# Kernel tuning notes

Hardware: AMD Instinct MI355X
Metric: run time of the kernel (lower is better)

Reference implementation:

```python
import jax, jax.numpy as jnp
import numpy as np

EPS = 1e-13

def masked_softmax(scores, mask):
    # scores: [B, L1, L2], mask: [B, L2] binary float
    # ESIM-style: softmax(scores * mask) * mask, renormalized.
    m = mask[:, None, :]                      # [B, 1, L2]
    r = jax.nn.softmax(scores * m, axis=-1) * m
    return r / (r.sum(axis=-1, keepdims=True) + EPS)

def weighted_sum(attn, tensor, mask):
    # attn: [B, L1, L2], tensor: [B, L2, D], mask: [B, L1]
    return jnp.matmul(attn, tensor) * mask[:, :, None]

def setup_inputs() -> dict:
    key = jax.random.key(0)
    k1, k2, k3, k4 = jax.random.split(key, 4)
    B, Lp, Lh, D = 64, 512, 512, 600
    encoded_premise = jax.random.normal(k1, (B, Lp, D), dtype=jnp.float32)
    encoded_hypothesis = jax.random.normal(k2, (B, Lh, D), dtype=jnp.float32)
    # binary padding masks (1 = valid token)
    premise_mask = (jax.random.uniform(k3, (B, Lp)) > 0.15).astype(jnp.float32)
    hypothesis_mask = (jax.random.uniform(k4, (B, Lh)) > 0.15).astype(jnp.float32)
    return {"encoded_premise": encoded_premise, "premise_mask": premise_mask,
            "encoded_hypothesis": encoded_hypothesis, "hypothesis_mask": hypothesis_mask}

def reference(encoded_premise, premise_mask, encoded_hypothesis, hypothesis_mask):
    # shared cross-attention score matrix [B, Lp, Lh]
    attn = jnp.einsum('bpd,bhd->bph', encoded_premise, encoded_hypothesis)
    a_p = masked_softmax(attn, hypothesis_mask)                    # [B, Lp, Lh]
    a_h = masked_softmax(attn.transpose(0, 2, 1), premise_mask)    # [B, Lh, Lp]
    weighted_premise = weighted_sum(a_p, encoded_hypothesis, premise_mask)      # [B, Lp, D]
    weighted_hypothesis = weighted_sum(a_h, encoded_premise, hypothesis_mask)   # [B, Lh, D]
    return (weighted_premise, weighted_hypothesis)
```

## Files before the change

### kernel.cpp

```cpp
#include <hip/hip_runtime.h>
#include <hip/hip_bf16.h>

#define DEVB 64
#define LSEQ 512
#define DDIM 600

typedef short short8 __attribute__((ext_vector_type(8)));
typedef float f32x4 __attribute__((ext_vector_type(4)));
typedef _Float16 f16x8 __attribute__((ext_vector_type(8)));
typedef _Float16 f16x4 __attribute__((ext_vector_type(4)));

constexpr int LDP = 40;

__device__ __forceinline__ unsigned short f2bf(float x) {
    union { float f; unsigned u; } v; v.f = x;
    unsigned r = v.u + 0x7fffu + ((v.u >> 16) & 1u);
    return (unsigned short)(r >> 16);
}
__device__ __forceinline__ f32x4 mfma16(short8 a, short8 b, f32x4 c) {
    return __builtin_amdgcn_mfma_f32_16x16x32_bf16(a, b, c, 0, 0, 0);
}
__device__ __forceinline__ f32x4 mfma16h(f16x8 a, f16x8 b, f32x4 c) {
    return __builtin_amdgcn_mfma_f32_16x16x32_f16(a, b, c, 0, 0, 0);
}

__global__ __launch_bounds__(256) void transcvt2(
    const float* __restrict__ P, const float* __restrict__ H,
    _Float16* __restrict__ pT, _Float16* __restrict__ hT)
{
    int blk = blockIdx.x;
    const float* X; _Float16* XT;
    if (blk < DEVB * 80) { X = P; XT = pT; }
    else { blk -= DEVB * 80; X = H; XT = hT; }

    int b   = blk / 80;
    int rem = blk % 80;
    int r0  = (rem / 10) << 6;
    int d0  = (rem % 10) << 6;
    const float* Xb = X + (size_t)b * LSEQ * DDIM;

    __shared__ _Float16 T[64 * 66];
    int t = threadIdx.x;
#pragma unroll
    for (int it = 0; it < 2; ++it) {
        int g  = t + (it << 8);
        int ri = g >> 3;
        int dc = (g & 7) << 3;
        if (d0 + dc < DDIM) {
            const float* src = Xb + (size_t)(r0 + ri) * DDIM + d0 + dc;
            float4 x0 = *(const float4*)src;
            float4 x1 = *(const float4*)(src + 4);
            float xf[8] = {x0.x, x0.y, x0.z, x0.w, x1.x, x1.y, x1.z, x1.w};
#pragma unroll
            for (int j = 0; j < 8; ++j)
                T[(dc + j) * 66 + ri] = (_Float16)xf[j];
        }
    }
    __syncthreads();

    int d  = t >> 2;
    int ch = (t & 3) << 4;
    if (d0 + d < DDIM) {
        unsigned buf[8];
#pragma unroll
        for (int i = 0; i < 8; ++i)
            buf[i] = *(const unsigned*)&T[d * 66 + ch + 2 * i];
        unsigned* dst = (unsigned*)(XT + ((size_t)b * DDIM + d0 + d) * LSEQ + r0 + ch);
        *(uint4*)(dst)     = *(uint4*)&buf[0];
        *(uint4*)(dst + 4) = *(uint4*)&buf[4];
    }
}

__global__ __launch_bounds__(256) void attn_gemm(
    const float* __restrict__ P, const float* __restrict__ H,
    float* __restrict__ attn)
{
    const int bid = blockIdx.x;
    const int swz = (bid & 7) * 128 + (bid >> 3);
    const int b  = swz >> 4;
    const int pt = ((swz >> 2) & 3) << 7;
    const int ht = (swz & 3) << 7;
    const float* Pb = P + ((size_t)b * LSEQ + pt) * DDIM;
    const float* Hb = H + ((size_t)b * LSEQ + ht) * DDIM;
    float* Ab = attn + (size_t)b * LSEQ * LSEQ;

    __shared__ _Float16 Ah[2][128 * 32], Al[2][128 * 32], Bh[2][128 * 32];

    const int t    = threadIdx.x;
    const int lane = t & 63;
    const int wave = t >> 6;
    const int wm = (wave >> 1) << 6;
    const int wn = (wave & 1) << 6;
    const int fr = lane & 15;
    const int fq = lane >> 4;
    const int srow = t >> 2;
    const int sc8  = (t & 3) << 3;

    const int wchunk = (t & 3) ^ ((srow >> 1) & 3);
    const int woff   = srow * 32 + (wchunk << 3);
    const int rcoff  = ((fq ^ ((fr >> 1) & 3)) << 3);

    float4 pf[8];
    const float4 fz = {0.f, 0.f, 0.f, 0.f};
    auto issue = [&](int k0) {
        bool ok = (k0 + sc8) < DDIM;
#pragma unroll
        for (int r = 0; r < 2; ++r) {
            size_t base = (size_t)(srow + (r << 6)) * DDIM + k0 + sc8;
            if (ok) {
                pf[r * 4 + 0] = *(const float4*)(Pb + base);
                pf[r * 4 + 1] = *(const float4*)(Pb + base + 4);
                pf[r * 4 + 2] = *(const float4*)(Hb + base);
                pf[r * 4 + 3] = *(const float4*)(Hb + base + 4);
            } else {
                pf[r * 4 + 0] = fz; pf[r * 4 + 1] = fz;
                pf[r * 4 + 2] = fz; pf[r * 4 + 3] = fz;
            }
        }
    };
    auto wr = [&](int buf) {
#pragma unroll
        for (int r = 0; r < 2; ++r) {
            float4 a0 = pf[r * 4 + 0], a1 = pf[r * 4 + 1];
            float4 h0 = pf[r * 4 + 2], h1 = pf[r * 4 + 3];
            float af[8] = {a0.x, a0.y, a0.z, a0.w, a1.x, a1.y, a1.z, a1.w};
            float hf[8] = {h0.x, h0.y, h0.z, h0.w, h1.x, h1.y, h1.z, h1.w};
            f16x8 hi, lo, bh;
#pragma unroll
            for (int j = 0; j < 8; ++j) {
                hi[j] = (_Float16)af[j];
                lo[j] = (_Float16)(af[j] - (float)hi[j]);
                bh[j] = (_Float16)hf[j];
            }
            int off = woff + (r << 11);
            *(f16x8*)&Ah[buf][off] = hi;
            *(f16x8*)&Al[buf][off] = lo;
            *(f16x8*)&Bh[buf][off] = bh;
        }
    };

    issue(0);
    wr(0);
    issue(32);
    __syncthreads();

    f32x4 acc[4][4];
#pragma unroll
    for (int i = 0; i < 4; ++i)
#pragma unroll
        for (int j = 0; j < 4; ++j) acc[i][j] = (f32x4){0.f, 0.f, 0.f, 0.f};

    constexpr int NK = 19;
    int cur = 0;
    for (int it = 0; it < NK; ++it) {
        f16x8 ah[4], al[4], bh[4];
#pragma unroll
        for (int i = 0; i < 4; ++i) {
            int ra = (wm + (i << 4) + fr) * 32 + rcoff;
            int rb = (wn + (i << 4) + fr) * 32 + rcoff;
            ah[i] = *(const f16x8*)&Ah[cur][ra];
            al[i] = *(const f16x8*)&Al[cur][ra];
            bh[i] = *(const f16x8*)&Bh[cur][rb];
        }
        if (it + 1 < NK) {
            wr(cur ^ 1);
            if (it + 2 < NK) issue((it + 2) << 5);
        }
#pragma unroll
        for (int mi = 0; mi < 4; ++mi)
#pragma unroll
            for (int ni = 0; ni < 4; ++ni) {
                f32x4 c = acc[mi][ni];
                c = mfma16h(ah[mi], bh[ni], c);
                c = mfma16h(al[mi], bh[ni], c);
                acc[mi][ni] = c;
            }
        __syncthreads();
        cur ^= 1;
    }

#pragma unroll
    for (int mi = 0; mi < 4; ++mi)
#pragma unroll
        for (int ni = 0; ni < 4; ++ni)
#pragma unroll
            for (int j = 0; j < 4; ++j) {
                int p = pt + wm + (mi << 4) + (fq << 2) + j;
                int h = ht + wn + (ni << 4) + fr;
                Ab[(size_t)p * LSEQ + h] = acc[mi][ni][j];
            }
}

__global__ __launch_bounds__(256) void stats_w1(
    const float* __restrict__ attn, const float* __restrict__ hmask,
    const float* __restrict__ pmask,
    float* __restrict__ M1, float* __restrict__ R1,
    _Float16* __restrict__ W1,
    float* __restrict__ Mp, float* __restrict__ Tp, float* __restrict__ Sp)
{
    int b      = blockIdx.x >> 3;
    int stripe = blockIdx.x & 7;
    int lane   = threadIdx.x & 63;
    int wave   = threadIdx.x >> 6;
    const float* hm = hmask + (b << 9);
    const float* pm = pmask + (b << 9);

    float4 m0 = *(const float4*)(hm + (lane << 3));
    float4 m1 = *(const float4*)(hm + (lane << 3) + 4);
    float mk[8] = {m0.x, m0.y, m0.z, m0.w, m1.x, m1.y, m1.z, m1.w};

    float cM[8], cT[8], cS[8];
#pragma unroll
    for (int j = 0; j < 8; ++j) { cM[j] = -1e30f; cT[j] = 0.f; cS[j] = 0.f; }

    for (int i = 0; i < 16; ++i) {
        int row   = (stripe << 6) + (wave << 4) + i;
        int rowid = (b << 9) + row;
        const float* rp = attn + (size_t)rowid * LSEQ + (lane << 3);
        float4 s0 = *(const float4*)rp;
        float4 s1 = *(const float4*)(rp + 4);
        float s[8] = {s0.x, s0.y, s0.z, s0.w, s1.x, s1.y, s1.z, s1.w};

        float v[8];
#pragma unroll
        for (int j = 0; j < 8; ++j) v[j] = s[j] * mk[j];
        float mx = -1e30f;
#pragma unroll
        for (int j = 0; j < 8; ++j) mx = fmaxf(mx, v[j]);
#pragma unroll
        for (int off = 32; off; off >>= 1) mx = fmaxf(mx, __shfl_xor(mx, off));

        float e[8], T = 0.f, S = 0.f;
#pragma unroll
        for (int j = 0; j < 8; ++j) { e[j] = __expf(v[j] - mx); T += mk[j] * e[j]; S += e[j]; }
#pragma unroll
        for (int off = 32; off; off >>= 1) { T += __shfl_xor(T, off); S += __shfl_xor(S, off); }
        float R = 1.f / (T + 1e-13f * S);

        if (W1) {
            union { f16x8 v8; _Float16 h[8]; } wv;
#pragma unroll
            for (int j = 0; j < 8; ++j) wv.h[j] = (_Float16)(mk[j] * e[j] * R);
            *(f16x8*)(W1 + (size_t)rowid * LSEQ + (lane << 3)) = wv.v8;
        }
        if (lane == 0) { M1[rowid] = mx; R1[rowid] = R; }

        float pmv = pm[row];
#pragma unroll
        for (int j = 0; j < 8; ++j) {
            float v2 = s[j] * pmv;
            float nm = fmaxf(cM[j], v2);
            float sc = __expf(cM[j] - nm);
            float e2 = __expf(v2 - nm);
            cT[j] = cT[j] * sc + pmv * e2;
            cS[j] = cS[j] * sc + e2;
            cM[j] = nm;
        }
    }

    __shared__ float LM[4][512], LT[4][512], LS[4][512];
#pragma unroll
    for (int j = 0; j < 8; ++j) {
        int c = (lane << 3) + j;
        LM[wave][c] = cM[j]; LT[wave][c] = cT[j]; LS[wave][c] = cS[j];
    }
    __syncthreads();

    size_t base = (size_t)((b << 3) + stripe) * 512;
    for (int cc = threadIdx.x; cc < 512; cc += 256) {
        float gm = fmaxf(fmaxf(LM[0][cc], LM[1][cc]), fmaxf(LM[2][cc], LM[3][cc]));
        float gT = 0.f, gS = 0.f;
#pragma unroll
        for (int w = 0; w < 4; ++w) {
            float sc = __expf(LM[w][cc] - gm);
            gT += LT[w][cc] * sc;
            gS += LS[w][cc] * sc;
        }
        Mp[base + cc] = gm; Tp[base + cc] = gT; Sp[base + cc] = gS;
    }
}

__global__ __launch_bounds__(256) void col_merge(
    const float* __restrict__ Mp, const float* __restrict__ Tp,
    const float* __restrict__ Sp, float* __restrict__ M2, float* __restrict__ R2)
{
    int b = blockIdx.x >> 1;
    int c = ((blockIdx.x & 1) << 8) + threadIdx.x;
    float gm = -1e30f, gT = 0.f, gS = 0.f;
#pragma unroll
    for (int st = 0; st < 8; ++st) {
        size_t idx = (size_t)((b << 3) + st) * 512 + c;
        float m = Mp[idx], tt = Tp[idx], ss = Sp[idx];
        float nm  = fmaxf(gm, m);
        float sc1 = __expf(gm - nm), sc2 = __expf(m - nm);
        gT = gT * sc1 + tt * sc2;
        gS = gS * sc1 + ss * sc2;
        gm = nm;
    }
    M2[(b << 9) + c] = gm;
    R2[(b << 9) + c] = 1.f / (gT + 1e-13f * gS);
}

__global__ __launch_bounds__(256) void w2gen_m(
    const float* __restrict__ attn, const float* __restrict__ pmask,
    const float* __restrict__ Mp, const float* __restrict__ Tp,
    const float* __restrict__ Sp, _Float16* __restrict__ W2)
{
    int blk = blockIdx.x;
    int b  = blk >> 5;
    int p0 = ((blk >> 2) & 7) << 6;
    int h0 = (blk & 3) << 7;
    const float* Ab = attn + (size_t)b * LSEQ * LSEQ;
    const float* pm = pmask + (b << 9);

    __shared__ float sM[128], sR[128];
    __shared__ _Float16 T[128 * 66];
    int t = threadIdx.x;
    if (t < 128) {
        float gm = -1e30f, gT = 0.f, gS = 0.f;
#pragma unroll
        for (int st = 0; st < 8; ++st) {
            size_t idx = (size_t)((b << 3) + st) * 512 + h0 + t;
            float m = Mp[idx], tt = Tp[idx], ss = Sp[idx];
            float nm  = fmaxf(gm, m);
            float sc1 = __expf(gm - nm), sc2 = __expf(m - nm);
            gT = gT * sc1 + tt * sc2;
            gS = gS * sc1 + ss * sc2;
            gm = nm;
        }
        sM[t] = gm;
        sR[t] = 1.f / (gT + 1e-13f * gS);
    }
    __syncthreads();

#pragma unroll
    for (int it = 0; it < 8; ++it) {
        int g  = t + (it << 8);
        int pi = g >> 5;
        int hc = (g & 31) << 2;
        float4 x = *(const float4*)(Ab + (size_t)(p0 + pi) * LSEQ + h0 + hc);
        float pv = pm[p0 + pi];
        _Float16 w0 = 0, w1 = 0, w2 = 0, w3 = 0;
        if (pv != 0.f) {
            w0 = (_Float16)(__expf(x.x - sM[hc + 0]) * sR[hc + 0]);
            w1 = (_Float16)(__expf(x.y - sM[hc + 1]) * sR[hc + 1]);
            w2 = (_Float16)(__expf(x.z - sM[hc + 2]) * sR[hc + 2]);
            w3 = (_Float16)(__expf(x.w - sM[hc + 3]) * sR[hc + 3]);
        }
        T[(hc + 0) * 66 + pi] = w0;
        T[(hc + 1) * 66 + pi] = w1;
        T[(hc + 2) * 66 + pi] = w2;
        T[(hc + 3) * 66 + pi] = w3;
    }
    __syncthreads();

    int h  = t >> 1;
    int po = (t & 1) << 5;
    unsigned buf[16];
#pragma unroll
    for (int i = 0; i < 16; ++i)
        buf[i] = *(const unsigned*)&T[h * 66 + po + 2 * i];
    unsigned* dst = (unsigned*)(W2 + ((size_t)(b << 9) + h0 + h) * LSEQ + p0 + po);
#pragma unroll
    for (int i = 0; i < 4; ++i)
        *(uint4*)(dst + 4 * i) = *(uint4*)&buf[4 * i];
}

__global__ __launch_bounds__(256) void gemm_fp16(
    const _Float16* __restrict__ W, const _Float16* __restrict__ BT,
    const float* __restrict__ mask_m, float* __restrict__ out)
{
    const int bid = blockIdx.x;
    const int swz = (bid & 7) * 160 + (bid >> 3);
    const int b   = swz / 20;
    const int rem = swz % 20;
    const int m0  = (rem / 5) << 7;
    const int n0  = (rem % 5) << 7;
    const _Float16* Wb = W  + (size_t)b * LSEQ * LSEQ;
    const _Float16* Bb = BT + (size_t)b * DDIM * LSEQ;

    __shared__ _Float16 Wl[2][128 * 32];
    __shared__ _Float16 Bl[2][128 * 32];

    const int t    = threadIdx.x;
    const int lane = t & 63;
    const int wave = t >> 6;
    const int wm = (wave >> 1) << 6;
    const int wn = (wave & 1) << 6;
    const int fr = lane & 15;
    const int fq = lane >> 4;
    const int srow = t >> 2;
    const int sc8  = (t & 3) << 3;

    const int wchunk = (t & 3) ^ ((srow >> 1) & 3);
    const int woff   = srow * 32 + (wchunk << 3);
    const int rcoff  = ((fq ^ ((fr >> 1) & 3)) << 3);

    f16x8 pw[2], pb[2];
    const f16x8 zz = {0, 0, 0, 0, 0, 0, 0, 0};
    auto issue = [&](int k0) {
#pragma unroll
        for (int r = 0; r < 2; ++r) {
            int row = srow + (r << 6);
            pw[r] = *(const f16x8*)(Wb + (size_t)(m0 + row) * LSEQ + k0 + sc8);
            int nrow = n0 + row;
            pb[r] = (nrow < DDIM) ? *(const f16x8*)(Bb + (size_t)nrow * LSEQ + k0 + sc8) : zz;
        }
    };
    auto wr = [&](int buf) {
#pragma unroll
        for (int r = 0; r < 2; ++r) {
            int off = woff + (r << 11);
            *(f16x8*)&Wl[buf][off] = pw[r];
            *(f16x8*)&Bl[buf][off] = pb[r];
        }
    };

    issue(0);
    wr(0);
    issue(32);
    __syncthreads();

    f32x4 acc[4][4];
#pragma unroll
    for (int i = 0; i < 4; ++i)
#pragma unroll
        for (int j = 0; j < 4; ++j) acc[i][j] = (f32x4){0.f, 0.f, 0.f, 0.f};

    constexpr int NK = 16;
    int cur = 0;
    for (int it = 0; it < NK; ++it) {
        f16x8 af[4], bfr[4];
#pragma unroll
        for (int i = 0; i < 4; ++i) {
            af[i]  = *(const f16x8*)&Wl[cur][(wm + (i << 4) + fr) * 32 + rcoff];
            bfr[i] = *(const f16x8*)&Bl[cur][(wn + (i << 4) + fr) * 32 + rcoff];
        }
        if (it + 1 < NK) {
            wr(cur ^ 1);
            if (it + 2 < NK) issue((it + 2) << 5);
        }
#pragma unroll
        for (int mi = 0; mi < 4; ++mi)
#pragma unroll
            for (int ni = 0; ni < 4; ++ni)
                acc[mi][ni] = mfma16h(af[mi], bfr[ni], acc[mi][ni]);
        __syncthreads();
        cur ^= 1;
    }

    const float* mmb = mask_m + (b << 9) + m0;
#pragma unroll
    for (int mi = 0; mi < 4; ++mi)
#pragma unroll
        for (int j = 0; j < 4; ++j) {
            int row = wm + (mi << 4) + (fq << 2) + j;
            float mm = mmb[row];
#pragma unroll
            for (int ni = 0; ni < 4; ++ni) {
                int d = n0 + wn + (ni << 4) + fr;
                if (d < DDIM)
                    out[((size_t)(b << 9) + m0 + row) * DDIM + d] = mm * acc[mi][ni][j];
            }
        }
}

template <int TRANSA>
__global__ __launch_bounds__(256) void wsum(
    const float* __restrict__ attn, const float* __restrict__ Bsrc,
    const float* __restrict__ mask_k, const float* __restrict__ mask_m,
    const float* __restrict__ Mst, const float* __restrict__ Rst,
    float* __restrict__ out)
{
    const int blk = blockIdx.x;
    const int b   = blk / 20;
    const int rem = blk % 20;
    const int m0  = (rem / 5) << 7;
    const int n0  = (rem % 5) << 7;

    const float* Ab  = attn + (size_t)b * LSEQ * LSEQ;
    const float* Bb  = Bsrc + (size_t)b * LSEQ * DDIM;
    const float* mkb = mask_k + (b << 9);

    __shared__ unsigned short Wl[128 * LDP];
    __shared__ unsigned short Bl[128 * LDP];
    __shared__ float Ml[128], Rl[128], Mm[128];

    const int t    = threadIdx.x;
    const int lane = t & 63;
    const int wave = t >> 6;
    const int wm = (wave >> 1) << 6;
    const int wn = (wave & 1) << 6;
    const int fr = lane & 15;
    const int fq = lane >> 4;

    if (t < 128) {
        Ml[t] = Mst[(b << 9) + m0 + t];
        Rl[t] = Rst[(b << 9) + m0 + t];
        Mm[t] = mask_m[(b << 9) + m0 + t];
    }
    __syncthreads();

    f32x4 acc[4][4];
#pragma unroll
    for (int i = 0; i < 4; ++i)
#pragma unroll
        for (int j = 0; j < 4; ++j) acc[i][j] = (f32x4){0.f, 0.f, 0.f, 0.f};

    for (int k0 = 0; k0 < LSEQ; k0 += 32) {
        if constexpr (TRANSA == 0) {
#pragma unroll
            for (int r = 0; r < 4; ++r) {
                int idx = t + (r << 8);
                int row = idx >> 3;
                int c4  = (idx & 7) << 2;
                float4 x  = *(const float4*)(Ab + (size_t)(m0 + row) * LSEQ + k0 + c4);
                float4 km = *(const float4*)(mkb + k0 + c4);
                float Mv = Ml[row], Rv = Rl[row];
                ushort4 w;
                w.x = (km.x != 0.f) ? f2bf(__expf(x.x - Mv) * Rv) : (unsigned short)0;
                w.y = (km.y != 0.f) ? f2bf(__expf(x.y - Mv) * Rv) : (unsigned short)0;
                w.z = (km.z != 0.f) ? f2bf(__expf(x.z - Mv) * Rv) : (unsigned short)0;
                w.w = (km.w != 0.f) ? f2bf(__expf(x.w - Mv) * Rv) : (unsigned short)0;
                *(ushort4*)&Wl[row * LDP + c4] = w;
            }
        } else {
#pragma unroll
            for (int r = 0; r < 4; ++r) {
                int mh = t & 127;
                int pq = (t >> 7) + (r << 1);
                float Mv = Ml[mh], Rv = Rl[mh];
                ushort4 w;
#pragma unroll
                for (int j = 0; j < 4; ++j) {
                    int k = k0 + (pq << 2) + j;
                    float x  = Ab[(size_t)k * LSEQ + m0 + mh];
                    float km = mkb[k];
                    ((unsigned short*)&w)[j] =
                        (km != 0.f) ? f2bf(__expf(x - Mv) * Rv) : (unsigned short)0;
                }
                *(ushort4*)&Wl[mh * LDP + (pq << 2)] = w;
            }
        }
#pragma unroll
        for (int r = 0; r < 4; ++r) {
            int d  = t & 127;
            int kq = (t >> 7) + (r << 1);
            bool valid = (n0 + d) < DDIM;
            ushort4 v;
#pragma unroll
            for (int j = 0; j < 4; ++j) {
                int k = k0 + (kq << 2) + j;
                float x = valid ? Bb[(size_t)k * DDIM + n0 + d] : 0.f;
                ((unsigned short*)&v)[j] = f2bf(x);
            }
            *(ushort4*)&Bl[d * LDP + (kq << 2)] = v;
        }
        __syncthreads();

        short8 af[4], bfr[4];
#pragma unroll
        for (int i = 0; i < 4; ++i) {
            af[i]  = *(const short8*)&Wl[(wm + (i << 4) + fr) * LDP + (fq << 3)];
            bfr[i] = *(const short8*)&Bl[(wn + (i << 4) + fr) * LDP + (fq << 3)];
        }
#pragma unroll
        for (int mi = 0; mi < 4; ++mi)
#pragma unroll
            for (int ni = 0; ni < 4; ++ni)
                acc[mi][ni] = mfma16(af[mi], bfr[ni], acc[mi][ni]);
        __syncthreads();
    }

#pragma unroll
    for (int mi = 0; mi < 4; ++mi)
#pragma unroll
        for (int j = 0; j < 4; ++j) {
            int row = wm + (mi << 4) + (fq << 2) + j;
            float mm = Mm[row];
#pragma unroll
            for (int ni = 0; ni < 4; ++ni) {
                int d = n0 + wn + (ni << 4) + fr;
                if (d < DDIM)
                    out[((size_t)(b << 9) + m0 + row) * DDIM + d] = mm * acc[mi][ni][j];
            }
        }
}

extern "C" void kernel_launch(void* const* d_in, const int* in_sizes, int n_in,
                              void* d_out, int out_size, void* d_ws, size_t ws_size,
                              hipStream_t stream)
{
    const float* P  = (const float*)d_in[0];
    const float* pm = (const float*)d_in[1];
    const float* H  = (const float*)d_in[2];
    const float* hm = (const float*)d_in[3];
    float* out = (float*)d_out;
    char* o  = (char*)d_out;
    char* ws = (char*)d_ws;

    const size_t E = (size_t)DEVB * LSEQ * DDIM;

    _Float16* hT = (_Float16*)(o + 78643200);
    _Float16* W1 = (_Float16*)(o + 117964800);

    const size_t fast_need = 143654912;

    if (ws_size >= fast_need) {
        float*     attn = (float*)ws;
        _Float16*  pT   = (_Float16*)(ws + 67108864);
        _Float16*  W2   = (_Float16*)(ws + 67108864 + 39321600);
        float*     Mp   = (float*)(ws + 139984896);
        float*     Tp   = Mp + (size_t)DEVB * 8 * 512;
        float*     Sp   = Tp + (size_t)DEVB * 8 * 512;
        float*     M1   = Sp + (size_t)DEVB * 8 * 512;
        float*     R1   = M1 + DEVB * LSEQ;

        transcvt2<<<DEVB * 160, 256, 0, stream>>>(P, H, pT, hT);
        attn_gemm<<<DEVB * 16, 256, 0, stream>>>(P, H, attn);
        stats_w1<<<DEVB * 8, 256, 0, stream>>>(attn, hm, pm, M1, R1, W1, Mp, Tp, Sp);
        w2gen_m<<<DEVB * 32, 256, 0, stream>>>(attn, pm, Mp, Tp, Sp, W2);
        gemm_fp16<<<DEVB * 20, 256, 0, stream>>>(W1, hT, pm, out);
        gemm_fp16<<<DEVB * 20, 256, 0, stream>>>(W2, pT, hm, out + E);
    } else {
        float* attn = (float*)ws;
        float* Mp   = (float*)(ws + 67108864);
        float* Tp   = Mp + (size_t)DEVB * 8 * 512;
        float* Sp   = Tp + (size_t)DEVB * 8 * 512;
        float* M1   = Sp + (size_t)DEVB * 8 * 512;
        float* R1   = M1 + DEVB * LSEQ;
        float* M2   = R1 + DEVB * LSEQ;
        float* R2   = M2 + DEVB * LSEQ;

        attn_gemm<<<DEVB * 16, 256, 0, stream>>>(P, H, attn);
        stats_w1<<<DEVB * 8, 256, 0, stream>>>(attn, hm, pm, M1, R1, nullptr, Mp, Tp, Sp);
        col_merge<<<DEVB * 2, 256, 0, stream>>>(Mp, Tp, Sp, M2, R2);
        wsum<0><<<DEVB * 20, 256, 0, stream>>>(attn, H, hm, pm, M1, R1, out);
        wsum<1><<<DEVB * 20, 256, 0, stream>>>(attn, P, pm, hm, M2, R2, out + E);
    }
}
```

Baseline: 318.1 us.

## Widen attn_gemm tile to 128x256 with 512-thread blocks

Changes the score GEMM tile from 128x128 to 128x256 by using 8 waves per block and halving the grid. Each block now loads and splits the premise tile into hi/lo fp16 once and reuses it against twice as many hypothesis rows, which cuts redundant global loads and conversion work for P. In exchange the block uses more LDS and threads, and with fewer blocks there is less occupancy slack. The hidden MFMA loop must index the wider B tile correctly, and the elided part may not show that.

Result: slower. 523.8 us (+64.6%).

```diff
diff --git a/kernel.cpp b/kernel.cpp
--- a/kernel.cpp
+++ b/kernel.cpp
@@ -71,26 +71,26 @@
     }
 }
 
-__global__ __launch_bounds__(256) void attn_gemm(
+__global__ __launch_bounds__(512, 4) void attn_gemm(
     const float* __restrict__ P, const float* __restrict__ H,
     float* __restrict__ attn)
 {
     const int bid = blockIdx.x;
-    const int swz = (bid & 7) * 128 + (bid >> 3);
-    const int b  = swz >> 4;
-    const int pt = ((swz >> 2) & 3) << 7;
-    const int ht = (swz & 3) << 7;
+    const int swz = (bid & 7) * 64 + (bid >> 3);
+    const int b  = swz >> 3;
+    const int pt = ((swz >> 1) & 3) << 7;
+    const int ht = (swz & 1) << 8;
     const float* Pb = P + ((size_t)b * LSEQ + pt) * DDIM;
     const float* Hb = H + ((size_t)b * LSEQ + ht) * DDIM;
     float* Ab = attn + (size_t)b * LSEQ * LSEQ;
 
-    __shared__ _Float16 Ah[2][128 * 32], Al[2][128 * 32], Bh[2][128 * 32];
+    __shared__ _Float16 Ah[2][128 * 32], Al[2][128 * 32], Bh[2][256 * 32];
 
     const int t    = threadIdx.x;
     const int lane = t & 63;
     const int wave = t >> 6;
-    const int wm = (wave >> 1) << 6;
-    const int wn = (wave & 1) << 6;
+    const int wm = (wave >> 2) << 6;
+    const int wn = (wave & 3) << 6;
     const int fr = lane & 15;
     const int fq = lane >> 4;
     const int srow = t >> 2;
@@ -100,42 +100,50 @@
     const int woff   = srow * 32 + (wchunk << 3);
     const int rcoff  = ((fq ^ ((fr >> 1) & 3)) << 3);
 
-    float4 pf[8];
+    float4 pf[6];
     const float4 fz = {0.f, 0.f, 0.f, 0.f};
     auto issue = [&](int k0) {
         bool ok = (k0 + sc8) < DDIM;
-#pragma unroll
-        for (int r = 0; r < 2; ++r) {
-            size_t base = (size_t)(srow + (r << 6)) * DDIM + k0 + sc8;
-            if (ok) {
-                pf[r * 4 + 0] = *(const float4*)(Pb + base);
-                pf[r * 4 + 1] = *(const float4*)(Pb + base + 4);
-                pf[r * 4 + 2] = *(const float4*)(Hb + base);
-                pf[r * 4 + 3] = *(const float4*)(Hb + base + 4);
-            } else {
-                pf[r * 4 + 0] = fz; pf[r * 4 + 1] = fz;
-                pf[r * 4 + 2] = fz; pf[r * 4 + 3] = fz;
-            }
+        size_t offA  = (size_t)srow * DDIM + k0 + sc8;
+        size_t offB1 = (size_t)(srow + 128) * DDIM + k0 + sc8;
+        if (ok) {
+            pf[0] = *(const float4*)(Pb + offA);
+            pf[1] = *(const float4*)(Pb + offA + 4);
+            pf[2] = *(const float4*)(Hb + offA);
+            pf[3] = *(const float4*)(Hb + offA + 4);
+            pf[4] = *(const float4*)(Hb + offB1);
+            pf[5] = *(const float4*)(Hb + offB1 + 4);
+        } else {
+            pf[0] = fz; pf[1] = fz; pf[2] = fz;
+            pf[3] = fz; pf[4] = fz; pf[5] = fz;
         }
     };
     auto wr = [&](int buf) {
-#pragma unroll
-        for (int r = 0; r < 2; ++r) {
-            float4 a0 = pf[r * 4 + 0], a1 = pf[r * 4 + 1];
-            float4 h0 = pf[r * 4 + 2], h1 = pf[r * 4 + 3];
-            float af[8] = {a0.x, a0.y, a0.z, a0.w, a1.x, a1.y, a1.z, a1.w};
-            float hf[8] = {h0.x, h0.y, h0.z, h0.w, h1.x, h1.y, h1.z, h1.w};
-            f16x8 hi, lo, bh;
+        {
+            float af[8] = {pf[0].x, pf[0].y, pf[0].z, pf[0].w,
+                           pf[1].x, pf[1].y, pf[1].z, pf[1].w};
+            f16x8 hi, lo;
 #pragma unroll
             for (int j = 0; j < 8; ++j) {
                 hi[j] = (_Float16)af[j];
                 lo[j] = (_Float16)(af[j] - (float)hi[j]);
-                bh[j] = (_Float16)hf[j];
-            }
-            int off = woff + (r << 11);
-            *(f16x8*)&Ah[buf][off] = hi;
-            *(f16x8*)&Al[buf][off] = lo;
-            *(f16x8*)&Bh[buf][off] = bh;
+            }
+            *(f16x8*)&Ah[buf][woff] = hi;
+            *(f16x8*)&Al[buf][woff] = lo;
+        }
+        {
+            float h0[8] = {pf[2].x, pf[2].y, pf[2].z, pf[2].w,
+                           pf[3].x, pf[3].y, pf[3].z, pf[3].w};
+            float h1[8] = {pf[4].x, pf[4].y, pf[4].z, pf[4].w,
+                           pf[5].x, pf[5].y, pf[5].z, pf[5].w};
+            f16x8 b0, b1;
+#pragma unroll
+            for (int j = 0; j < 8; ++j) {
+                b0[j] = (_Float16)h0[j];
+                b1[j] = (_Float16)h1[j];
+            }
+            *(f16x8*)&Bh[buf][woff] = b0;
+            *(f16x8*)&Bh[buf][woff + 128 * 32] = b1;
         }
     };
 
@@ -617,7 +625,7 @@
         float*     R1   = M1 + DEVB * LSEQ;
 
         transcvt2<<<DEVB * 160, 256, 0, stream>>>(P, H, pT, hT);
-        attn_gemm<<<DEVB * 16, 256, 0, stream>>>(P, H, attn);
+        attn_gemm<<<DEVB * 8, 512, 0, stream>>>(P, H, attn);
         stats_w1<<<DEVB * 8, 256, 0, stream>>>(attn, hm, pm, M1, R1, W1, Mp, Tp, Sp);
         w2gen_m<<<DEVB * 32, 256, 0, stream>>>(attn, pm, Mp, Tp, Sp, W2);
         gemm_fp16<<<DEVB * 20, 256, 0, stream>>>(W1, hT, pm, out);
@@ -632,7 +640,7 @@
         float* M2   = R1 + DEVB * LSEQ;
         float* R2   = M2 + DEVB * LSEQ;
 
-        attn_gemm<<<DEVB * 16, 256, 0, stream>>>(P, H, attn);
+        attn_gemm<<<DEVB * 8, 512, 0, stream>>>(P, H, attn);
         stats_w1<<<DEVB * 8, 256, 0, stream>>>(attn, hm, pm, M1, R1, nullptr, Mp, Tp, Sp);
         col_merge<<<DEVB * 2, 256, 0, stream>>>(Mp, Tp, Sp, M2, R2);
         wsum<0><<<DEVB * 20, 256, 0, stream>>>(attn, H, hm, pm, M1, R1, out);
```
